# Kernel optimization log

Measured on AMD Instinct MI355X. Metric: run time of the kernel, lower is better.

Reference implementation:

```python
import jax, jax.numpy as jnp
import numpy as np

N, IN_DIM, D, H, E_DIM, G, NPG = 512, 16, 256, 8, 6, 32, 16
C = D           # per-head channels in GATv2Conv/TransformerConv (out_channels=d_model)
HD = D // H     # MultiheadAttention head dim


def _ln(x, g, b, eps=1e-5):
    m = jnp.mean(x, -1, keepdims=True)
    v = jnp.mean((x - m) ** 2, -1, keepdims=True)
    return (x - m) * jax.lax.rsqrt(v + eps) * g + b


def _seg_softmax(logits, seg, n):
    # numerically stable softmax over edges grouped by destination node
    m = jax.ops.segment_max(logits, seg, num_segments=n)
    m = jnp.where(jnp.isfinite(m), m, 0.0)
    e = jnp.exp(logits - m[seg])
    s = jax.ops.segment_sum(e, seg, num_segments=n)
    return e / jnp.maximum(s[seg], 1e-16)


def _forward(x, edge_attr, emb_w, emb_b, emb_g, emb_bb, pe, gat_lw, gat_lb, gat_rw, gat_rb, gat_ew, gat_att, gat_bias, tq_w, tq_b, tk_w, tk_b, tv_w, tv_b, te_w, tskip_w, tskip_b, tbeta_w, ln_g, ln_b, mha_in_w, mha_in_b, mha_out_w, mha_out_b, pool_w, pool_b, c1_w, c1_b, c1_g, c1_bb, rb_w, rb_b, rb_g, rb_bb, c2_w, c2_b, edge_index, batch):
    src, dst = edge_index[0], edge_index[1]
    E = edge_attr.shape[0]
    # input embedding (Linear + LayerNorm) + learned positional encoding (eval: no dropout)
    h = _ln(x @ emb_w.T + emb_b, emb_g, emb_bb) + pe[:N]
    residual = h
    # --- GATv2Conv(d_model, d_model, heads=H, edge_dim=6, concat=False, add_self_loops=False) ---
    xl = (h @ gat_lw.T + gat_lb).reshape(N, H, C)          # source transform
    xr = (h @ gat_rw.T + gat_rb).reshape(N, H, C)          # target transform
    ee = (edge_attr @ gat_ew.T).reshape(E, H, C)
    z = jax.nn.leaky_relu(xl[src] + xr[dst] + ee, 0.2)
    a = _seg_softmax(jnp.einsum('ehc,hc->eh', z, gat_att), dst, N)
    x_gat = jax.ops.segment_sum(xl[src] * a[..., None], dst, num_segments=N).mean(1) + gat_bias
    x_gat = _ln(x_gat, ln_g, ln_b)
    # --- TransformerConv(d_model, d_model, heads=H, edge_dim=6, concat=False, beta=True) ---
    te = (edge_attr @ te_w.T).reshape(E, H, C)
    q = (x_gat @ tq_w.T + tq_b).reshape(N, H, C)[dst]
    k = (x_gat @ tk_w.T + tk_b).reshape(N, H, C)[src] + te
    v = (x_gat @ tv_w.T + tv_b).reshape(N, H, C)[src] + te
    a2 = _seg_softmax((q * k).sum(-1) / np.sqrt(C).astype(np.float32), dst, N)
    out = jax.ops.segment_sum(v * a2[..., None], dst, num_segments=N).mean(1)
    r = x_gat @ tskip_w.T + tskip_b
    beta = jax.nn.sigmoid(jnp.concatenate([out, r, out - r], -1) @ tbeta_w.T)
    x_tr = _ln(beta * r + (1.0 - beta) * out, ln_g, ln_b)
    # --- dynamic attention mask: after the repeat/permute/reshape gymnastics this equals
    #     ds[:N] repeated H*N times, reshaped to [H, N, N] ---
    im = edge_attr[:, 5]
    ds = jnp.exp(-0.5 * ((im - 125.09) / 15.0) ** 2)
    ds = 1.0 - (ds - ds.min()) / (ds.max() - ds.min())
    mask = jnp.repeat(ds[:N], H * N).reshape(H, N, N)
    # --- cross MultiheadAttention (query=x_tr, key=x_gat, value=h, attn_mask added) ---
    wq, wk, wv = jnp.split(mha_in_w, 3, axis=0)
    bq, bk, bv = jnp.split(mha_in_b, 3, axis=0)
    qh = ((x_tr @ wq.T + bq) / np.sqrt(HD).astype(np.float32)).reshape(N, H, HD).transpose(1, 0, 2)
    kh = (x_gat @ wk.T + bk).reshape(N, H, HD).transpose(1, 0, 2)
    vh = (h @ wv.T + bv).reshape(N, H, HD).transpose(1, 0, 2)
    attn = jax.nn.softmax(qh @ kh.transpose(0, 2, 1) + mask, axis=-1)   # [H,N,N]
    o = (attn @ vh).transpose(1, 0, 2).reshape(N, D) @ mha_out_w.T + mha_out_b
    # torch broadcast of [N,1,D] attn output + [N,D] residual -> [N,N,D]
    x3 = o[:, None, :] + residual[None, :, :]
    # attention pooling: softmax over a size-1 dim yields all-ones scores (kept faithfully)
    x2 = x3.reshape(N * N, D)
    brep = jnp.tile(batch, N)
    score = jax.nn.softmax(x2 @ pool_w.T + pool_b, axis=1)
    pooled = jax.ops.segment_sum(score * x2, brep, num_segments=G)
    # classifier: Linear->LN->GELU->ResidualBlockv2->Linear (dropout off in eval)
    c = jax.nn.gelu(_ln(pooled @ c1_w.T + c1_b, c1_g, c1_bb), approximate=False)
    c = c + jax.nn.gelu(_ln(c @ rb_w.T + rb_b, rb_g, rb_bb), approximate=False)
    return c @ c2_w.T + c2_b   # [G, 1]


def setup_inputs():
    key = jax.random.key(0)
    ks = iter(jax.random.split(key, 64))
    f = lambda *sh: 0.02 * jax.random.normal(next(ks), sh, jnp.float32)
    # G fully-connected directed cliques of NPG nodes (no self loops) -> every node has in-edges
    i = np.arange(NPG)
    s, t = np.meshgrid(i, i, indexing='ij')
    msk = s != t
    s, t = s[msk], t[msk]
    off = (np.arange(G) * NPG)[:, None]
    edge_index = jnp.asarray(np.stack([(s[None] + off).reshape(-1), (t[None] + off).reshape(-1)]), jnp.int32)
    E = edge_index.shape[1]
    batch = jnp.asarray(np.repeat(np.arange(G), NPG), jnp.int32)
    x = jax.random.normal(next(ks), (N, IN_DIM), jnp.float32)
    edge_attr = jax.random.normal(next(ks), (E, E_DIM), jnp.float32)
    edge_attr = edge_attr.at[:, 5].set(edge_attr[:, 5] * 30.0 + 125.0)  # invariant-mass-like column
    HC = H * C
    return dict(
        x=x, edge_attr=edge_attr,
        emb_w=f(D, IN_DIM), emb_b=f(D), emb_g=jnp.ones(D), emb_bb=jnp.zeros(D),
        pe=f(1000, D),
        gat_lw=f(HC, D), gat_lb=f(HC), gat_rw=f(HC, D), gat_rb=f(HC),
        gat_ew=f(HC, E_DIM), gat_att=f(H, C), gat_bias=f(C),
        tq_w=f(HC, D), tq_b=f(HC), tk_w=f(HC, D), tk_b=f(HC),
        tv_w=f(HC, D), tv_b=f(HC), te_w=f(HC, E_DIM),
        tskip_w=f(D, D), tskip_b=f(D), tbeta_w=f(1, 3 * D),
        ln_g=jnp.ones(D), ln_b=jnp.zeros(D),
        mha_in_w=f(3 * D, D), mha_in_b=f(3 * D), mha_out_w=f(D, D), mha_out_b=f(D),
        pool_w=f(1, D), pool_b=f(1),
        c1_w=f(128, D), c1_b=f(128), c1_g=jnp.ones(128), c1_bb=jnp.zeros(128),
        rb_w=f(128, 128), rb_b=f(128), rb_g=jnp.ones(128), rb_bb=jnp.zeros(128),
        c2_w=f(1, 128), c2_b=f(1),
        edge_index=edge_index, batch=batch)


def reference(x, edge_attr, emb_w, emb_b, emb_g, emb_bb, pe, gat_lw, gat_lb, gat_rw, gat_rb, gat_ew, gat_att, gat_bias, tq_w, tq_b, tk_w, tk_b, tv_w, tv_b, te_w, tskip_w, tskip_b, tbeta_w, ln_g, ln_b, mha_in_w, mha_in_b, mha_out_w, mha_out_b, pool_w, pool_b, c1_w, c1_b, c1_g, c1_bb, rb_w, rb_b, rb_g, rb_bb, c2_w, c2_b, edge_index, batch):
    return _forward(x, edge_attr, emb_w, emb_b, emb_g, emb_bb, pe, gat_lw, gat_lb, gat_rw, gat_rb, gat_ew, gat_att, gat_bias, tq_w, tq_b, tk_w, tk_b, tv_w, tv_b, te_w, tskip_w, tskip_b, tbeta_w, ln_g, ln_b, mha_in_w, mha_in_b, mha_out_w, mha_out_b, pool_w, pool_b, c1_w, c1_b, c1_g, c1_bb, rb_w, rb_b, rb_g, rb_bb, c2_w, c2_b, edge_index, batch)
```

## Files before the change

kernel.cpp:

```cpp
#include <hip/hip_runtime.h>
#include <hip/hip_bf16.h>
#include <math.h>

#define NN 512
#define DM 256
#define NH 8
#define NG 32
#define NPG 16
#define INDIM 16
#define BIGW (2048 * 256)

typedef __hip_bfloat16 bf16;
typedef __attribute__((ext_vector_type(8))) short short8;
typedef __attribute__((ext_vector_type(4))) float f32x4;

__device__ __forceinline__ float b2f(bf16 v) { return __bfloat162float(v); }
__device__ __forceinline__ bf16 f2b(float v) { return __float2bfloat16(v); }
__device__ __forceinline__ short f2bs(float v) { bf16 t = __float2bfloat16(v); return *(short*)&t; }
__device__ __forceinline__ float fin(float v) {
    return (v == v && v > -1e30f && v < 1e30f) ? v : 0.f;
}
__device__ __forceinline__ int is_bf16(const void* ones_arr) {
    return ((const unsigned short*)ones_arr)[0] == 0x3F80u;
}

__device__ __forceinline__ void unpack8(uint4 u, float* w) {
    unsigned uu[4] = {u.x, u.y, u.z, u.w};
    #pragma unroll
    for (int j = 0; j < 4; j++) {
        __hip_bfloat162 b2 = *reinterpret_cast<const __hip_bfloat162*>(&uu[j]);
        float2 f = __bfloat1622float2(b2);
        w[2 * j] = f.x; w[2 * j + 1] = f.y;
    }
}
__device__ __forceinline__ float4 bload4(const bf16* p) {
    uint2 u = *(const uint2*)p;
    __hip_bfloat162 a = *reinterpret_cast<const __hip_bfloat162*>(&u.x);
    __hip_bfloat162 b = *reinterpret_cast<const __hip_bfloat162*>(&u.y);
    float2 f0 = __bfloat1622float2(a), f1 = __bfloat1622float2(b);
    return make_float4(f0.x, f0.y, f1.x, f1.y);
}

__device__ __forceinline__ float dot256(const float* xrow, const bf16* wrow) {
    const uint4* w4 = (const uint4*)wrow;
    uint4 q = w4[0];
    float acc = 0.f;
    for (int k8 = 0; k8 < 32; k8++) {
        uint4 qn = w4[(k8 + 1) & 31];
        float w[8]; unpack8(q, w);
        const float4* sp = (const float4*)&xrow[k8 * 8];
        float4 a0 = sp[0], a1 = sp[1];
        acc += a0.x*w[0] + a0.y*w[1] + a0.z*w[2] + a0.w*w[3]
             + a1.x*w[4] + a1.y*w[5] + a1.z*w[6] + a1.w*w[7];
        q = qn;
    }
    return acc;
}

template<int BS>
__device__ __forceinline__ float ln_norm(float v, float g, float b, float* red) {
    int t = threadIdx.x;
    red[t] = v; __syncthreads();
    for (int s = BS / 2; s > 0; s >>= 1) { if (t < s) red[t] += red[t + s]; __syncthreads(); }
    float mean = red[0] * (1.0f / (float)BS); __syncthreads();
    float d = v - mean;
    red[t] = d * d; __syncthreads();
    for (int s = BS / 2; s > 0; s >>= 1) { if (t < s) red[t] += red[t + s]; __syncthreads(); }
    float var = red[0] * (1.0f / (float)BS); __syncthreads();
    return d * rsqrtf(var + 1e-5f) * g + b;
}

struct CvtTab { const void* p[35]; int cum[36]; };
__global__ void k_convert(CvtTab tab, const void* ones, bf16* wbuf, float* gz, int nz) {
    int i = blockIdx.x * 256 + threadIdx.x;
    if (i < tab.cum[35]) {
        int bf = is_bf16(ones);
        int a = 0;
        while (i >= tab.cum[a + 1]) a++;
        int off = i - tab.cum[a];
        float v = bf ? b2f(((const bf16*)tab.p[a])[off]) : ((const float*)tab.p[a])[off];
        wbuf[i] = f2b(v);
    } else if (i < tab.cum[35] + nz) {
        gz[i - tab.cum[35]] = 0.f;
    }
}

struct Cvt5 { const void* p[5]; };
__global__ void k_convert_big(Cvt5 tab, const void* ones, bf16* wbig) {
    int i = blockIdx.x * 256 + threadIdx.x;
    int a = blockIdx.y;
    int bf = is_bf16(ones);
    float v = bf ? b2f(((const bf16*)tab.p[a])[i]) : ((const float*)tab.p[a])[i];
    wbig[(size_t)a * BIGW + i] = f2b(v);
}

__global__ void k_embed(const bf16* xw, const bf16* emw, const bf16* emb, const bf16* emg,
                        const bf16* embb, const bf16* pe, float* h,
                        float* pre1, float* pre2, float* gsum_h) {
    int n = blockIdx.x, t = threadIdx.x;
    size_t gi = (size_t)n * DM + t;
    pre1[gi] = 0.f;
    pre2[gi] = 0.f;
    __shared__ float xin[INDIM];
    __shared__ float red[DM];
    if (t < INDIM) xin[t] = b2f(xw[n * INDIM + t]);
    __syncthreads();
    float acc = b2f(emb[t]);
    #pragma unroll
    for (int k = 0; k < INDIM; k++) acc += xin[k] * b2f(emw[t * INDIM + k]);
    float y = ln_norm<DM>(acc, b2f(emg[t]), b2f(embb[t]), red);
    float hv = fin(y + b2f(pe[gi]));
    h[gi] = hv;
    atomicAdd(&gsum_h[(n >> 4) * DM + t], hv);
}

__device__ __forceinline__ void row_softmax16(float* M, int tid) {
    if (tid < NPG) {
        float* row = M + tid * NPG;
        float m = -1e30f;
        #pragma unroll
        for (int s = 0; s < NPG; s++) m = fmaxf(m, row[s]);
        if (m < -1e29f) {
            #pragma unroll
            for (int s = 0; s < NPG; s++) row[s] = 0.f;
        } else {
            float sum = 0.f;
            #pragma unroll
            for (int s = 0; s < NPG; s++) sum += expf(row[s] - m);
            float inv = 1.f / fmaxf(sum, 1e-16f);
            #pragma unroll
            for (int s = 0; s < NPG; s++) row[s] = expf(row[s] - m) * inv;
        }
    }
}

__global__ __launch_bounds__(512, 1)
void k_gat_fused(const float* h, const bf16* lw, const bf16* rw,
                 const bf16* lb, const bf16* rbv, const bf16* eww, const bf16* attw,
                 const bf16* ea, const int* src, const int* dst, int epg, float* pre) {
    extern __shared__ char smraw[];
    int g = blockIdx.x, hh = blockIdx.y, tid = threadIdx.x;
    bf16* hb     = (bf16*)smraw;
    bf16* ew_s   = hb + NPG * DM;
    bf16* att_s  = ew_s + 6 * DM;
    float* ea_s  = (float*)(att_s + DM);
    float* Mx    = ea_s + 6 * epg;
    int* sl_s    = (int*)(Mx + NPG * NPG);
    int* dl_s    = sl_s + epg;
    bf16* xl_s   = (bf16*)(dl_s + epg);
    bf16* xr_s   = xl_s + NPG * DM;

    int ebase = g * epg;
    for (int i = tid; i < NPG * DM; i += 512) hb[i] = f2b(h[(size_t)g * NPG * DM + i]);
    for (int i = tid; i < 6 * DM; i += 512) {
        int f = i >> 8, cc = i & 255;
        ew_s[f * DM + cc] = eww[(size_t)(hh * DM + cc) * 6 + f];
    }
    if (tid < DM) att_s[tid] = attw[hh * DM + tid];
    for (int i = tid; i < 6 * epg; i += 512) {
        int f = i / epg, e = i - f * epg;
        ea_s[f * epg + e] = b2f(ea[(size_t)(ebase + e) * 6 + f]);
    }
    if (tid < NPG * NPG) Mx[tid] = -1e30f;
    if (tid < epg) {
        int e = ebase + tid;
        sl_s[tid] = (src[e] - g * NPG) & (NPG - 1);
        dl_s[tid] = (dst[e] - g * NPG) & (NPG - 1);
    }
    __syncthreads();

    int lane = tid & 63, wave = tid >> 6;
    int n16 = lane & 15, quad = lane >> 4;
    f32x4 accA[2], accB[2];
    #pragma unroll
    for (int ct = 0; ct < 2; ct++) { accA[ct] = (f32x4)0.f; accB[ct] = (f32x4)0.f; }
    for (int ks = 0; ks < 8; ks++) {
        short8 a8 = *(const short8*)&hb[n16 * DM + ks * 32 + quad * 8];
        #pragma unroll
        for (int ct = 0; ct < 2; ct++) {
            int col = (ct * 8 + wave) * 16 + n16;
            size_t wo = (size_t)(hh * DM + col) * DM + ks * 32 + quad * 8;
            short8 bL = *(const short8*)(lw + wo);
            short8 bR = *(const short8*)(rw + wo);
            accA[ct] = __builtin_amdgcn_mfma_f32_16x16x32_bf16(a8, bL, accA[ct], 0, 0, 0);
            accB[ct] = __builtin_amdgcn_mfma_f32_16x16x32_bf16(a8, bR, accB[ct], 0, 0, 0);
        }
    }
    #pragma unroll
    for (int ct = 0; ct < 2; ct++) {
        int col = (ct * 8 + wave) * 16 + n16;
        float blv = b2f(lb[hh * DM + col]), brv = b2f(rbv[hh * DM + col]);
        #pragma unroll
        for (int reg = 0; reg < 4; reg++) {
            int row = quad * 4 + reg;
            xl_s[row * DM + col] = f2b(accA[ct][reg] + blv);
            xr_s[row * DM + col] = f2b(accB[ct][reg] + brv);
        }
    }
    __syncthreads();

    int c4 = lane * 4;
    for (int ei = wave; ei < epg; ei += 8) {
        int sl = sl_s[ei], dl = dl_s[ei];
        float ee0 = 0.f, ee1 = 0.f, ee2 = 0.f, ee3 = 0.f;
        #pragma unroll
        for (int f = 0; f < 6; f++) {
            float eb = ea_s[f * epg + ei];
            float4 wf = bload4(&ew_s[f * DM + c4]);
            ee0 += eb * wf.x; ee1 += eb * wf.y; ee2 += eb * wf.z; ee3 += eb * wf.w;
        }
        float4 av = bload4(&att_s[c4]);
        float4 xlv = bload4(&xl_s[sl * DM + c4]);
        float4 xrv = bload4(&xr_s[dl * DM + c4]);
        float z0 = xlv.x + xrv.x + ee0;
        float z1 = xlv.y + xrv.y + ee1;
        float z2 = xlv.z + xrv.z + ee2;
        float z3 = xlv.w + xrv.w + ee3;
        z0 = (z0 >= 0.f) ? z0 : 0.2f * z0;
        z1 = (z1 >= 0.f) ? z1 : 0.2f * z1;
        z2 = (z2 >= 0.f) ? z2 : 0.2f * z2;
        z3 = (z3 >= 0.f) ? z3 : 0.2f * z3;
        float acc = z0 * av.x + z1 * av.y + z2 * av.z + z3 * av.w;
        #pragma unroll
        for (int off = 32; off > 0; off >>= 1) acc += __shfl_down(acc, off);
        if (lane == 0) Mx[dl * NPG + sl] = fin(acc);
    }
    __syncthreads();
    row_softmax16(Mx, tid);
    __syncthreads();

    int c = tid & 255, halfd = tid >> 8;
    float xlv[NPG];
    #pragma unroll
    for (int s = 0; s < NPG; s++) xlv[s] = b2f(xl_s[s * DM + c]);
    #pragma unroll
    for (int dd = 0; dd < 8; dd++) {
        int d = halfd * 8 + dd;
        const float* Ar = Mx + d * NPG;
        float acc = 0.f;
        #pragma unroll
        for (int s = 0; s < NPG; s++) acc += Ar[s] * xlv[s];
        atomicAdd(&pre[(size_t)(g * NPG + d) * DM + c], fin(acc));
    }
}

__global__ void k_gat_post_skip(const float* pre, const bf16* gat_bias, const bf16* lng,
                                const bf16* lnb, const bf16* skw, const bf16* skb,
                                float* x_gat, float* rbuf) {
    int n = blockIdx.x, t = threadIdx.x;
    __shared__ float red[DM];
    __shared__ float xrow[DM];
    float v = pre[(size_t)n * DM + t] * 0.125f + b2f(gat_bias[t]);
    float y = fin(ln_norm<DM>(v, b2f(lng[t]), b2f(lnb[t]), red));
    x_gat[(size_t)n * DM + t] = y;
    xrow[t] = y;
    __syncthreads();
    rbuf[(size_t)n * DM + t] = fin(dot256(xrow, skw + (size_t)t * DM) + b2f(skb[t]));
}

__global__ __launch_bounds__(512, 1)
void k_tr_fused(const float* xg, const bf16* qw, const bf16* kw, const bf16* vw,
                const bf16* qb, const bf16* kb, const bf16* vb, const bf16* tew,
                const bf16* ea, const int* src, const int* dst, int epg, float* pre) {
    extern __shared__ char smraw[];
    int g = blockIdx.x, hh = blockIdx.y, tid = threadIdx.x;
    bf16* hb    = (bf16*)smraw;
    bf16* tw_s  = hb + NPG * DM;
    float* ea_s = (float*)(tw_s + 6 * DM);
    float* Lqk  = ea_s + 6 * epg;
    float* Mx   = Lqk + NPG * NPG;
    float* P    = Mx + NPG * NPG;
    float* W6   = P + NPG * 6;
    int* emap   = (int*)(W6 + NPG * 6);
    int* sl_s   = emap + NPG * NPG;
    int* dl_s   = sl_s + epg;
    bf16* q_s   = (bf16*)(dl_s + epg);
    bf16* k_s   = q_s + NPG * DM;
    bf16* v_s   = k_s + NPG * DM;

    int ebase = g * epg;
    for (int i = tid; i < NPG * DM; i += 512) hb[i] = f2b(xg[(size_t)g * NPG * DM + i]);
    for (int i = tid; i < 6 * DM; i += 512) {
        int f = i >> 8, cc = i & 255;
        tw_s[f * DM + cc] = tew[(size_t)(hh * DM + cc) * 6 + f];
    }
    for (int i = tid; i < 6 * epg; i += 512) {
        int f = i / epg, e = i - f * epg;
        ea_s[f * epg + e] = b2f(ea[(size_t)(ebase + e) * 6 + f]);
    }
    if (tid < NPG * NPG) { Mx[tid] = -1e30f; emap[tid] = -1; }
    if (tid < epg) {
        int e = ebase + tid;
        sl_s[tid] = (src[e] - g * NPG) & (NPG - 1);
        dl_s[tid] = (dst[e] - g * NPG) & (NPG - 1);
    }
    __syncthreads();

    int lane = tid & 63, wave = tid >> 6;
    int n16 = lane & 15, quad = lane >> 4;
    f32x4 aQ[2], aK[2], aV[2];
    #pragma unroll
    for (int ct = 0; ct < 2; ct++) { aQ[ct] = (f32x4)0.f; aK[ct] = (f32x4)0.f; aV[ct] = (f32x4)0.f; }
    for (int ks = 0; ks < 8; ks++) {
        short8 a8 = *(const short8*)&hb[n16 * DM + ks * 32 + quad * 8];
        #pragma unroll
        for (int ct = 0; ct < 2; ct++) {
            int col = (ct * 8 + wave) * 16 + n16;
            size_t wo = (size_t)(hh * DM + col) * DM + ks * 32 + quad * 8;
            short8 bQ = *(const short8*)(qw + wo);
            short8 bK = *(const short8*)(kw + wo);
            short8 bV = *(const short8*)(vw + wo);
            aQ[ct] = __builtin_amdgcn_mfma_f32_16x16x32_bf16(a8, bQ, aQ[ct], 0, 0, 0);
            aK[ct] = __builtin_amdgcn_mfma_f32_16x16x32_bf16(a8, bK, aK[ct], 0, 0, 0);
            aV[ct] = __builtin_amdgcn_mfma_f32_16x16x32_bf16(a8, bV, aV[ct], 0, 0, 0);
        }
    }
    #pragma unroll
    for (int ct = 0; ct < 2; ct++) {
        int col = (ct * 8 + wave) * 16 + n16;
        float bq = b2f(qb[hh * DM + col]), bk = b2f(kb[hh * DM + col]), bv = b2f(vb[hh * DM + col]);
        #pragma unroll
        for (int reg = 0; reg < 4; reg++) {
            int row = quad * 4 + reg;
            q_s[row * DM + col] = f2b(aQ[ct][reg] + bq);
            k_s[row * DM + col] = f2b(aK[ct][reg] + bk);
            v_s[row * DM + col] = f2b(aV[ct][reg] + bv);
        }
    }
    __syncthreads();

    if (wave == 0) {
        f32x4 acc = (f32x4)0.f;
        for (int ks = 0; ks < 8; ks++) {
            short8 a8 = *(const short8*)&q_s[n16 * DM + ks * 32 + quad * 8];
            short8 b8 = *(const short8*)&k_s[n16 * DM + ks * 32 + quad * 8];
            acc = __builtin_amdgcn_mfma_f32_16x16x32_bf16(a8, b8, acc, 0, 0, 0);
        }
        #pragma unroll
        for (int reg = 0; reg < 4; reg++)
            Lqk[(quad * 4 + reg) * NPG + n16] = acc[reg];
    } else if (wave <= 2) {
        int idx = tid - 64;
        if (idx < NPG * 6) {
            int d = idx / 6, f = idx - d * 6;
            const bf16* qr = q_s + d * DM;
            const bf16* twr = tw_s + f * DM;
            float acc = 0.f;
            for (int cc = 0; cc < DM; cc += 4) {
                float4 qv = bload4(qr + cc);
                float4 t4 = bload4(twr + cc);
                acc += qv.x * t4.x + qv.y * t4.y + qv.z * t4.z + qv.w * t4.w;
            }
            P[idx] = acc;
        }
    }
    __syncthreads();

    if (tid < epg) {
        int sl = sl_s[tid], dl = dl_s[tid];
        float acc = Lqk[dl * NPG + sl];
        #pragma unroll
        for (int f = 0; f < 6; f++) acc += ea_s[f * epg + tid] * P[dl * 6 + f];
        Mx[dl * NPG + sl] = fin(acc * 0.0625f);
        emap[dl * NPG + sl] = tid;
    }
    __syncthreads();
    row_softmax16(Mx, tid);
    __syncthreads();
    if (tid < NPG * 6) {
        int d = tid / 6, f = tid - d * 6;
        float acc = 0.f;
        #pragma unroll
        for (int s = 0; s < NPG; s++) {
            int e = emap[d * NPG + s];
            if (e >= 0) acc += Mx[d * NPG + s] * ea_s[f * epg + e];
        }
        W6[tid] = acc;
    }
    __syncthreads();

    int c = tid & 255, halfd = tid >> 8;
    float vv[NPG];
    #pragma unroll
    for (int s = 0; s < NPG; s++) vv[s] = b2f(v_s[s * DM + c]);
    float twc[6];
    #pragma unroll
    for (int f = 0; f < 6; f++) twc[f] = b2f(tw_s[f * DM + c]);
    #pragma unroll
    for (int dd = 0; dd < 8; dd++) {
        int d = halfd * 8 + dd;
        const float* Ar = Mx + d * NPG;
        const float* Wr = W6 + d * 6;
        float acc = 0.f;
        #pragma unroll
        for (int s = 0; s < NPG; s++) acc += Ar[s] * vv[s];
        #pragma unroll
        for (int f = 0; f < 6; f++) acc += Wr[f] * twc[f];
        atomicAdd(&pre[(size_t)(g * NPG + d) * DM + c], fin(acc));
    }
}

__global__ void k_tr_post_qkv(const float* pre, const float* rbuf, const float* x_gat,
                              const float* h, const bf16* tbeta, const bf16* lng,
                              const bf16* lnb, const bf16* mw, const bf16* mb, float* qkv) {
    int n = blockIdx.x, t = threadIdx.x;
    __shared__ float red[DM];
    __shared__ float xtr_s[DM];
    __shared__ float xg_s[DM];
    __shared__ float h_s[DM];
    __shared__ float beta_sh;
    float outc = pre[(size_t)n * DM + t] * 0.125f;
    float rc = rbuf[(size_t)n * DM + t];
    xg_s[t] = x_gat[(size_t)n * DM + t];
    h_s[t] = h[(size_t)n * DM + t];
    float w1 = b2f(tbeta[t]), w2 = b2f(tbeta[DM + t]), w3 = b2f(tbeta[2 * DM + t]);
    red[t] = outc * (w1 + w3) + rc * (w2 - w3);
    __syncthreads();
    for (int s2 = 128; s2 > 0; s2 >>= 1) { if (t < s2) red[t] += red[t + s2]; __syncthreads(); }
    if (t == 0) beta_sh = 1.0f / (1.0f + expf(-red[0]));
    __syncthreads();
    float beta = beta_sh;
    float mix = beta * rc + (1.0f - beta) * outc;
    float y = fin(ln_norm<DM>(mix, b2f(lng[t]), b2f(lnb[t]), red));
    xtr_s[t] = y;
    __syncthreads();
    float q = (dot256(xtr_s, mw + (size_t)t * DM) + b2f(mb[t])) * 0.17677669529663689f;
    float k = dot256(xg_s, mw + (size_t)(DM + t) * DM) + b2f(mb[DM + t]);
    float v = dot256(h_s, mw + (size_t)(2 * DM + t) * DM) + b2f(mb[2 * DM + t]);
    qkv[(size_t)n * DM + t] = fin(q);
    qkv[((size_t)NN + n) * DM + t] = fin(k);
    qkv[((size_t)2 * NN + n) * DM + t] = fin(v);
}

#define KPAD 40
#define SPAD 516
__global__ __launch_bounds__(256, 1)
void k_attn(const float* qh, const float* kh, const float* vh, float* ao) {
    extern __shared__ char sm[];
    bf16* qb   = (bf16*)sm;
    bf16* KV   = qb + 16 * 32;
    float* Sc  = (float*)(KV + 256 * KPAD);
    float* Op  = Sc + 16 * SPAD;
    float* red = Op + 4 * 16 * 32;
    int qt = blockIdx.x, hd = blockIdx.y, tid = threadIdx.x;
    int lane = tid & 63, wave = tid >> 6, n16 = lane & 15, quad = lane >> 4;

    for (int i = tid; i < 16 * 32; i += 256)
        qb[i] = f2b(qh[(size_t)(qt * 16 + (i >> 5)) * DM + hd * 32 + (i & 31)]);

    for (int half = 0; half < 2; half++) {
        __syncthreads();
        for (int i = tid; i < 256 * 32; i += 256) {
            int j = i >> 5, d = i & 31;
            KV[j * KPAD + d] = f2b(kh[(size_t)(half * 256 + j) * DM + hd * 32 + d]);
        }
        __syncthreads();
        short8 a8 = *(const short8*)&qb[n16 * 32 + quad * 8];
        #pragma unroll
        for (int it = 0; it < 4; it++) {
            int ktl = wave * 4 + it;
            short8 b8 = *(const short8*)&KV[(ktl * 16 + n16) * KPAD + quad * 8];
            f32x4 acc = (f32x4)0.f;
            acc = __builtin_amdgcn_mfma_f32_16x16x32_bf16(a8, b8, acc, 0, 0, 0);
            #pragma unroll
            for (int reg = 0; reg < 4; reg++)
                Sc[(quad * 4 + reg) * SPAD + half * 256 + ktl * 16 + n16] = acc[reg];
        }
    }
    __syncthreads();

    int r = tid >> 4, li = tid & 15;
    float m = -1e30f;
    for (int s = 0; s < 32; s++) m = fmaxf(m, Sc[r * SPAD + li + 16 * s]);
    red[r * 16 + li] = m; __syncthreads();
    for (int st = 8; st > 0; st >>= 1) {
        if (li < st) red[r * 16 + li] = fmaxf(red[r * 16 + li], red[r * 16 + li + st]);
        __syncthreads();
    }
    m = red[r * 16];
    __syncthreads();
    float sum = 0.f;
    for (int s = 0; s < 32; s++) sum += expf(Sc[r * SPAD + li + 16 * s] - m);
    red[r * 16 + li] = sum; __syncthreads();
    for (int st = 8; st > 0; st >>= 1) {
        if (li < st) red[r * 16 + li] += red[r * 16 + li + st];
        __syncthreads();
    }
    float inv = 1.0f / fmaxf(red[r * 16], 1e-16f);
    for (int s = 0; s < 32; s++) {
        int idx = r * SPAD + li + 16 * s;
        Sc[idx] = expf(Sc[idx] - m) * inv;
    }

    f32x4 o0 = (f32x4)0.f, o1 = (f32x4)0.f;
    for (int half = 0; half < 2; half++) {
        __syncthreads();
        for (int i = tid; i < 256 * 32; i += 256) {
            int j = i >> 5, d = i & 31;
            KV[j * KPAD + d] = f2b(vh[(size_t)(half * 256 + j) * DM + hd * 32 + d]);
        }
        __syncthreads();
        #pragma unroll
        for (int it = 0; it < 2; it++) {
            int ksl = wave * 2 + it;
            int ks = half * 8 + ksl;
            const float* sp = &Sc[n16 * SPAD + ks * 32 + quad * 8];
            float4 s0 = *(const float4*)sp, s1 = *((const float4*)sp + 1);
            short8 a8;
            a8[0] = f2bs(s0.x); a8[1] = f2bs(s0.y); a8[2] = f2bs(s0.z); a8[3] = f2bs(s0.w);
            a8[4] = f2bs(s1.x); a8[5] = f2bs(s1.y); a8[6] = f2bs(s1.z); a8[7] = f2bs(s1.w);
            short8 bv0, bv1;
            #pragma unroll
            for (int j = 0; j < 8; j++) {
                bf16 t0 = KV[(ksl * 32 + quad * 8 + j) * KPAD + n16];
                bf16 t1 = KV[(ksl * 32 + quad * 8 + j) * KPAD + 16 + n16];
                bv0[j] = *(short*)&t0;
                bv1[j] = *(short*)&t1;
            }
            o0 = __builtin_amdgcn_mfma_f32_16x16x32_bf16(a8, bv0, o0, 0, 0, 0);
            o1 = __builtin_amdgcn_mfma_f32_16x16x32_bf16(a8, bv1, o1, 0, 0, 0);
        }
    }
    #pragma unroll
    for (int reg = 0; reg < 4; reg++) {
        Op[wave * 512 + (quad * 4 + reg) * 32 + n16] = o0[reg];
        Op[wave * 512 + (quad * 4 + reg) * 32 + 16 + n16] = o1[reg];
    }
    __syncthreads();
    for (int e = tid; e < 512; e += 256) {
        float v = Op[e] + Op[512 + e] + Op[1024 + e] + Op[1536 + e];
        ao[(size_t)(qt * 16 + (e >> 5)) * DM + hd * 32 + (e & 31)] = fin(v);
    }
}

__global__ void k_outproj(const float* ao, const bf16* W, const bf16* B,
                          float* obuf, float* gsum_o) {
    int n = blockIdx.x, t = threadIdx.x;
    __shared__ float xrow[DM];
    xrow[t] = ao[(size_t)n * DM + t];
    __syncthreads();
    float v = fin(dot256(xrow, W + (size_t)t * DM) + b2f(B[t]));
    obuf[(size_t)n * DM + t] = v;
    atomicAdd(&gsum_o[(n >> 4) * DM + t], v);
}

__global__ void k_mlp(const float* gsum_o, const float* gsum_h,
                      const bf16* c1_w, const bf16* c1_b, const bf16* c1_g,
                      const bf16* c1_bb, const bf16* rb_w, const bf16* rb_b,
                      const bf16* rb_g, const bf16* rb_bb, const bf16* c2_w,
                      const bf16* c2_b, const void* ones, void* out) {
    int g = blockIdx.x, t = threadIdx.x;
    __shared__ float pl[DM];
    __shared__ float u[128];
    __shared__ float red[128];
    float os0 = 0.f, os1 = 0.f;
    #pragma unroll
    for (int b = 0; b < NG; b++) {
        os0 += gsum_o[b * DM + t];
        os1 += gsum_o[b * DM + t + 128];
    }
    pl[t]       = fin((float)NPG * os0 + (float)NN * gsum_h[g * DM + t]);
    pl[t + 128] = fin((float)NPG * os1 + (float)NN * gsum_h[g * DM + t + 128]);
    __syncthreads();
    float acc = dot256(pl, c1_w + (size_t)t * DM) + b2f(c1_b[t]);
    float y = ln_norm<128>(acc, b2f(c1_g[t]), b2f(c1_bb[t]), red);
    float gl = 0.5f * y * (1.0f + erff(y * 0.70710678118654752f));
    u[t] = gl; __syncthreads();
    float acc2 = b2f(rb_b[t]);
    for (int k = 0; k < 128; k++) acc2 += u[k] * b2f(rb_w[(size_t)t * 128 + k]);
    float y2 = ln_norm<128>(acc2, b2f(rb_g[t]), b2f(rb_bb[t]), red);
    float cfin = gl + 0.5f * y2 * (1.0f + erff(y2 * 0.70710678118654752f));
    red[t] = cfin * b2f(c2_w[t]);
    __syncthreads();
    for (int s2 = 64; s2 > 0; s2 >>= 1) { if (t < s2) red[t] += red[t + s2]; __syncthreads(); }
    if (t == 0) {
        float res = fin(red[0] + b2f(c2_b[0]));
        if (is_bf16(ones)) ((bf16*)out)[g] = f2b(res);
        else               ((float*)out)[g] = res;
    }
}

extern "C" void kernel_launch(void* const* d_in, const int* in_sizes, int n_in,
                              void* d_out, int out_size, void* d_ws, size_t ws_size,
                              hipStream_t stream) {
    const int E = in_sizes[1] / 6;
    const int epg = E / NG;
    const int* eidx = (const int*)d_in[42];
    const int* srcp = eidx;
    const int* dstp = eidx + E;
    const void* ones = d_in[4];

    static const int idxs[35] = {0,1,2,3,4,5,6,8,10,11,12,13,15,17,19,20,21,22,23,24,
                                 25,26,27,28,29,32,33,34,35,36,37,38,39,40,41};
    CvtTab tab;
    int wOff[44];
    int cum = 0;
    for (int a = 0; a < 35; a++) {
        tab.p[a] = d_in[idxs[a]];
        tab.cum[a] = cum;
        wOff[idxs[a]] = cum;
        cum += in_sizes[idxs[a]];
    }
    tab.cum[35] = cum;
    const int totalW = cum;
    Cvt5 tab5;
    tab5.p[0] = d_in[7];  tab5.p[1] = d_in[9];
    tab5.p[2] = d_in[14]; tab5.p[3] = d_in[16]; tab5.p[4] = d_in[18];

    bf16* wbuf = (bf16*)d_ws;
    size_t wbytes = ((size_t)totalW * 2 + 255) & ~(size_t)255;
    float* fb = (float*)((char*)d_ws + wbytes);
    const size_t SL = (size_t)NN * DM;
    float* h      = fb;
    float* x_gat  = fb + SL;
    float* rbuf   = fb + 2 * SL;
    float* pre1   = fb + 3 * SL;
    float* pre2   = fb + 4 * SL;
    float* qkv    = fb + 5 * SL;
    float* gsum_o = fb + 8 * SL;
    float* gsum_h = gsum_o + NG * DM;
    bf16* wbig = (bf16*)qkv;
    float* ao = pre1;
    float* obuf = pre2;
    const int NZ = 2 * NG * DM;

    #define WB(i) (wbuf + wOff[i])

    k_convert<<<(totalW + NZ + 255) / 256, 256, 0, stream>>>(tab, ones, wbuf, gsum_o, NZ);
    k_convert_big<<<dim3(BIGW / 256, 5), 256, 0, stream>>>(tab5, ones, wbig);

    k_embed<<<NN, DM, 0, stream>>>(WB(0), WB(2), WB(3), WB(4), WB(5), WB(6), h,
                                   pre1, pre2, gsum_h);

    int gat_lds = NPG*DM*2 + 6*DM*2 + DM*2 + (6*epg + NPG*NPG + 2*epg) * 4
                + 2*NPG*DM*2 + 16;
    k_gat_fused<<<dim3(NG, NH), 512, gat_lds, stream>>>(
        h, wbig, wbig + BIGW, WB(8), WB(10), WB(11), WB(12), WB(1), srcp, dstp, epg, pre1);
    k_gat_post_skip<<<NN, DM, 0, stream>>>(pre1, WB(13), WB(24), WB(25), WB(21), WB(22),
                                           x_gat, rbuf);

    int tr_lds = NPG*DM*2 + 6*DM*2 + (6*epg + 2*NPG*NPG + 2*NPG*6) * 4
               + (NPG*NPG + 2*epg) * 4 + 3*NPG*DM*2 + 16;
    k_tr_fused<<<dim3(NG, NH), 512, tr_lds, stream>>>(
        x_gat, wbig + 2 * (size_t)BIGW, wbig + 3 * (size_t)BIGW, wbig + 4 * (size_t)BIGW,
        WB(15), WB(17), WB(19), WB(20), WB(1), srcp, dstp, epg, pre2);
    k_tr_post_qkv<<<NN, DM, 0, stream>>>(pre2, rbuf, x_gat, h, WB(23), WB(24), WB(25),
                                         WB(26), WB(27), qkv);

    int attn_lds = 16*32*2 + 256*KPAD*2 + 16*SPAD*4 + 4*16*32*4 + 16*16*4;
    k_attn<<<dim3(NN / 16, NH), 256, attn_lds, stream>>>(qkv, qkv + SL, qkv + 2 * SL, ao);
    k_outproj<<<NN, DM, 0, stream>>>(ao, WB(28), WB(29), obuf, gsum_o);

    k_mlp<<<NG, 128, 0, stream>>>(gsum_o, gsum_h, WB(32), WB(33), WB(34), WB(35),
                                  WB(36), WB(37), WB(38), WB(39), WB(40), WB(41),
                                  ones, d_out);
    #undef WB
}
```

Measured before the change: 304.3 us.

## Pre-swizzle weights into MFMA fragment layout, fuse convert kernels, swizzle attention LDS

The large projection weights are now permuted during conversion into an MFMA-fragment order, so each wave's short8 B-operand loads in the GAT and Transformer kernels become contiguous 16-byte chunks instead of strided row reads. The two conversion kernels are merged into one launch over a 6-row grid. In the attention kernel, K and V tiles are written to LDS in fragment order, which replaces the per-element gathers for the V operand with single vector loads. The Q fragment is also loaded directly into registers instead of being staged through LDS. The cost is more scattered stores during conversion and during LDS fills.

```diff
diff --git a/kernel.cpp b/kernel.cpp
--- a/kernel.cpp
+++ b/kernel.cpp
@@ -71,27 +71,32 @@
 }
 
 struct CvtTab { const void* p[35]; int cum[36]; };
-__global__ void k_convert(CvtTab tab, const void* ones, bf16* wbuf, float* gz, int nz) {
-    int i = blockIdx.x * 256 + threadIdx.x;
-    if (i < tab.cum[35]) {
-        int bf = is_bf16(ones);
-        int a = 0;
-        while (i >= tab.cum[a + 1]) a++;
-        int off = i - tab.cum[a];
-        float v = bf ? b2f(((const bf16*)tab.p[a])[off]) : ((const float*)tab.p[a])[off];
-        wbuf[i] = f2b(v);
-    } else if (i < tab.cum[35] + nz) {
-        gz[i - tab.cum[35]] = 0.f;
-    }
-}
-
 struct Cvt5 { const void* p[5]; };
-__global__ void k_convert_big(Cvt5 tab, const void* ones, bf16* wbig) {
+__global__ void k_convert_all(Cvt5 tab5, CvtTab tab, const void* ones, bf16* wbig,
+                              bf16* wbuf, float* gz, int nz) {
     int i = blockIdx.x * 256 + threadIdx.x;
     int a = blockIdx.y;
     int bf = is_bf16(ones);
-    float v = bf ? b2f(((const bf16*)tab.p[a])[i]) : ((const float*)tab.p[a])[i];
-    wbig[(size_t)a * BIGW + i] = f2b(v);
+    if (a < 5) {
+        if (i >= BIGW) return;
+        float v = bf ? b2f(((const bf16*)tab5.p[a])[i]) : ((const float*)tab5.p[a])[i];
+        int row = i >> 8, k = i & 255;
+        int hh = row >> 8, col = row & 255;
+        int T = col >> 4, n16 = col & 15;
+        int ks = k >> 5, quad = (k >> 3) & 3, j = k & 7;
+        int dst = ((((hh * 16 + T) * 8 + ks) * 4 + quad) * 16 + n16) * 8 + j;
+        wbig[(size_t)a * BIGW + dst] = f2b(v);
+    } else {
+        if (i < tab.cum[35]) {
+            int aa = 0;
+            while (i >= tab.cum[aa + 1]) aa++;
+            int off = i - tab.cum[aa];
+            float v = bf ? b2f(((const bf16*)tab.p[aa])[off]) : ((const float*)tab.p[aa])[off];
+            wbuf[i] = f2b(v);
+        } else if (i < tab.cum[35] + nz) {
+            gz[i - tab.cum[35]] = 0.f;
+        }
+    }
 }
 
 __global__ void k_embed(const bf16* xw, const bf16* emw, const bf16* emb, const bf16* emg,
@@ -178,10 +183,10 @@
         short8 a8 = *(const short8*)&hb[n16 * DM + ks * 32 + quad * 8];
         #pragma unroll
         for (int ct = 0; ct < 2; ct++) {
-            int col = (ct * 8 + wave) * 16 + n16;
-            size_t wo = (size_t)(hh * DM + col) * DM + ks * 32 + quad * 8;
-            short8 bL = *(const short8*)(lw + wo);
-            short8 bR = *(const short8*)(rw + wo);
+            int T = ct * 8 + wave;
+            size_t fo = (((size_t)(hh * 16 + T) * 8 + ks) * 4 + quad) * 128 + n16 * 8;
+            short8 bL = *(const short8*)(lw + fo);
+            short8 bR = *(const short8*)(rw + fo);
             accA[ct] = __builtin_amdgcn_mfma_f32_16x16x32_bf16(a8, bL, accA[ct], 0, 0, 0);
             accB[ct] = __builtin_amdgcn_mfma_f32_16x16x32_bf16(a8, bR, accB[ct], 0, 0, 0);
         }
@@ -305,11 +310,11 @@
         short8 a8 = *(const short8*)&hb[n16 * DM + ks * 32 + quad * 8];
         #pragma unroll
         for (int ct = 0; ct < 2; ct++) {
-            int col = (ct * 8 + wave) * 16 + n16;
-            size_t wo = (size_t)(hh * DM + col) * DM + ks * 32 + quad * 8;
-            short8 bQ = *(const short8*)(qw + wo);
-            short8 bK = *(const short8*)(kw + wo);
-            short8 bV = *(const short8*)(vw + wo);
+            int T = ct * 8 + wave;
+            size_t fo = (((size_t)(hh * 16 + T) * 8 + ks) * 4 + quad) * 128 + n16 * 8;
+            short8 bQ = *(const short8*)(qw + fo);
+            short8 bK = *(const short8*)(kw + fo);
+            short8 bV = *(const short8*)(vw + fo);
             aQ[ct] = __builtin_amdgcn_mfma_f32_16x16x32_bf16(a8, bQ, aQ[ct], 0, 0, 0);
             aK[ct] = __builtin_amdgcn_mfma_f32_16x16x32_bf16(a8, bK, aK[ct], 0, 0, 0);
             aV[ct] = __builtin_amdgcn_mfma_f32_16x16x32_bf16(a8, bV, aV[ct], 0, 0, 0);
@@ -432,36 +437,40 @@
     qkv[((size_t)2 * NN + n) * DM + t] = fin(v);
 }
 
-#define KPAD 40
 #define SPAD 516
 __global__ __launch_bounds__(256, 1)
 void k_attn(const float* qh, const float* kh, const float* vh, float* ao) {
     extern __shared__ char sm[];
-    bf16* qb   = (bf16*)sm;
-    bf16* KV   = qb + 16 * 32;
-    float* Sc  = (float*)(KV + 256 * KPAD);
+    bf16* KF   = (bf16*)sm;
+    float* Sc  = (float*)(KF + 8192);
     float* Op  = Sc + 16 * SPAD;
     float* red = Op + 4 * 16 * 32;
     int qt = blockIdx.x, hd = blockIdx.y, tid = threadIdx.x;
     int lane = tid & 63, wave = tid >> 6, n16 = lane & 15, quad = lane >> 4;
 
-    for (int i = tid; i < 16 * 32; i += 256)
-        qb[i] = f2b(qh[(size_t)(qt * 16 + (i >> 5)) * DM + hd * 32 + (i & 31)]);
+    short8 a8q;
+    {
+        const float* qp = &qh[(size_t)(qt * 16 + n16) * DM + hd * 32 + quad * 8];
+        float4 q0 = *(const float4*)qp, q1 = *((const float4*)qp + 1);
+        a8q[0] = f2bs(q0.x); a8q[1] = f2bs(q0.y); a8q[2] = f2bs(q0.z); a8q[3] = f2bs(q0.w);
+        a8q[4] = f2bs(q1.x); a8q[5] = f2bs(q1.y); a8q[6] = f2bs(q1.z); a8q[7] = f2bs(q1.w);
+    }
 
     for (int half = 0; half < 2; half++) {
         __syncthreads();
-        for (int i = tid; i < 256 * 32; i += 256) {
-            int j = i >> 5, d = i & 31;
-            KV[j * KPAD + d] = f2b(kh[(size_t)(half * 256 + j) * DM + hd * 32 + d]);
+        for (int i = tid; i < 8192; i += 256) {
+            int jj = i >> 5, d = i & 31;
+            bf16 val = f2b(kh[(size_t)(half * 256 + jj) * DM + hd * 32 + d]);
+            int ktl = jj >> 4, nn = jj & 15, qd = d >> 3, j8 = d & 7;
+            KF[((ktl * 4 + qd) * 16 + nn) * 8 + j8] = val;
         }
         __syncthreads();
-        short8 a8 = *(const short8*)&qb[n16 * 32 + quad * 8];
         #pragma unroll
         for (int it = 0; it < 4; it++) {
             int ktl = wave * 4 + it;
-            short8 b8 = *(const short8*)&KV[(ktl * 16 + n16) * KPAD + quad * 8];
+            short8 b8 = *(const short8*)&KF[((ktl * 4 + quad) * 16 + n16) * 8];
             f32x4 acc = (f32x4)0.f;
-            acc = __builtin_amdgcn_mfma_f32_16x16x32_bf16(a8, b8, acc, 0, 0, 0);
+            acc = __builtin_amdgcn_mfma_f32_16x16x32_bf16(a8q, b8, acc, 0, 0, 0);
             #pragma unroll
             for (int reg = 0; reg < 4; reg++)
                 Sc[(quad * 4 + reg) * SPAD + half * 256 + ktl * 16 + n16] = acc[reg];
@@ -495,9 +504,12 @@
     f32x4 o0 = (f32x4)0.f, o1 = (f32x4)0.f;
     for (int half = 0; half < 2; half++) {
         __syncthreads();
-        for (int i = tid; i < 256 * 32; i += 256) {
-            int j = i >> 5, d = i & 31;
-            KV[j * KPAD + d] = f2b(vh[(size_t)(half * 256 + j) * DM + hd * 32 + d]);
+        for (int i = tid; i < 8192; i += 256) {
+            int jj = i >> 5, d = i & 31;
+            bf16 val = f2b(vh[(size_t)(half * 256 + jj) * DM + hd * 32 + d]);
+            int ksl = jj >> 5, kin = jj & 31, qd = kin >> 3, j8 = kin & 7;
+            int nn = d & 15, which = d >> 4;
+            KF[which * 4096 + ((ksl * 4 + qd) * 16 + nn) * 8 + j8] = val;
         }
         __syncthreads();
         #pragma unroll
@@ -509,14 +521,8 @@
             short8 a8;
             a8[0] = f2bs(s0.x); a8[1] = f2bs(s0.y); a8[2] = f2bs(s0.z); a8[3] = f2bs(s0.w);
             a8[4] = f2bs(s1.x); a8[5] = f2bs(s1.y); a8[6] = f2bs(s1.z); a8[7] = f2bs(s1.w);
-            short8 bv0, bv1;
-            #pragma unroll
-            for (int j = 0; j < 8; j++) {
-                bf16 t0 = KV[(ksl * 32 + quad * 8 + j) * KPAD + n16];
-                bf16 t1 = KV[(ksl * 32 + quad * 8 + j) * KPAD + 16 + n16];
-                bv0[j] = *(short*)&t0;
-                bv1[j] = *(short*)&t1;
-            }
+            short8 bv0 = *(const short8*)&KF[((ksl * 4 + quad) * 16 + n16) * 8];
+            short8 bv1 = *(const short8*)&KF[4096 + ((ksl * 4 + quad) * 16 + n16) * 8];
             o0 = __builtin_amdgcn_mfma_f32_16x16x32_bf16(a8, bv0, o0, 0, 0, 0);
             o1 = __builtin_amdgcn_mfma_f32_16x16x32_bf16(a8, bv1, o1, 0, 0, 0);
         }
@@ -626,8 +632,10 @@
 
     #define WB(i) (wbuf + wOff[i])
 
-    k_convert<<<(totalW + NZ + 255) / 256, 256, 0, stream>>>(tab, ones, wbuf, gsum_o, NZ);
-    k_convert_big<<<dim3(BIGW / 256, 5), 256, 0, stream>>>(tab5, ones, wbig);
+    int gx_small = (totalW + NZ + 255) / 256;
+    int gx = BIGW / 256;
+    if (gx_small > gx) gx = gx_small;
+    k_convert_all<<<dim3(gx, 6), 256, 0, stream>>>(tab5, tab, ones, wbig, wbuf, gsum_o, NZ);
 
     k_embed<<<NN, DM, 0, stream>>>(WB(0), WB(2), WB(3), WB(4), WB(5), WB(6), h,
                                    pre1, pre2, gsum_h);
@@ -647,7 +655,7 @@
     k_tr_post_qkv<<<NN, DM, 0, stream>>>(pre2, rbuf, x_gat, h, WB(23), WB(24), WB(25),
                                          WB(26), WB(27), qkv);
 
-    int attn_lds = 16*32*2 + 256*KPAD*2 + 16*SPAD*4 + 4*16*32*4 + 16*16*4;
+    int attn_lds = 8192 * 2 + (16 * SPAD + 4 * 16 * 32 + 16 * 16) * 4;
     k_attn<<<dim3(NN / 16, NH), 256, attn_lds, stream>>>(qkv, qkv + SL, qkv + 2 * SL, ao);
     k_outproj<<<NN, DM, 0, stream>>>(ao, WB(28), WB(29), obuf, gsum_o);
 
```

Measured after the change: 295.7 us. -2.8%, faster.
